# Kernel tuning notes

Measured on AMD Instinct MI355X. Metric: run time of the kernel, lower is better.

The kernel has to match this reference:

```python
import jax, jax.numpy as jnp
import numpy as np

N, E, DIN, DH, DC = 50000, 1600000, 128, 128, 40
EPS = 1e-5  # BatchNorm eps


def _seg_sum(v, idx, n):
    return jax.ops.segment_sum(v, idx, num_segments=n)


def setup_inputs() -> dict:
    key = jax.random.key(0)
    ks = jax.random.split(key, 24)
    rn = lambda i, shp, s=0.05: jax.random.normal(ks[i], shp, jnp.float32) * s
    return {
        "x": jax.random.normal(ks[0], (N, DIN), jnp.float32),
        "src": jax.random.randint(ks[1], (E,), 0, N, jnp.int32),
        "dst": jax.random.randint(ks[2], (E,), 0, N, jnp.int32),
        # CoNet layer 1 (in -> hidden)
        "w11s": rn(3, (DIN, DH)), "w11n": rn(4, (DIN, DH)), "b11": jnp.zeros((DH,), jnp.float32),
        "w12": rn(5, (DIN, DH)), "b12": jnp.zeros((DH,), jnp.float32),
        "w13": rn(6, (DIN, DH)), "a13l": rn(7, (DH,)), "a13r": rn(8, (DH,)), "b13": jnp.zeros((DH,), jnp.float32),
        "cw1": jax.random.uniform(ks[9], (3,), jnp.float32, 0.5, 1.5),
        # BatchNorm1d
        "g": jnp.ones((DH,), jnp.float32), "be": jnp.zeros((DH,), jnp.float32),
        # CoNet layer 2 (hidden -> out)
        "w21s": rn(10, (DH, DC)), "w21n": rn(11, (DH, DC)), "b21": jnp.zeros((DC,), jnp.float32),
        "w22": rn(12, (DH, DC)), "b22": jnp.zeros((DC,), jnp.float32),
        "w23": rn(13, (DH, DC)), "a23l": rn(14, (DC,)), "a23r": rn(15, (DC,)), "b23": jnp.zeros((DC,), jnp.float32),
        "cw2": jax.random.uniform(ks[16], (3,), jnp.float32, 0.5, 1.5),
    }


def conet(x, src, dst, ws, wn, bs, wg, bg, wa, al, ar, ba, cw):
    """AFFN CoNet: SAGE(mean) + GCN + GAT(1 head), fused by normalized weights."""
    n = x.shape[0]
    ones = jnp.ones((src.shape[0],), x.dtype)
    indeg = _seg_sum(ones, dst, n)   # in-degree per node
    outdeg = _seg_sum(ones, src, n)  # out-degree per node

    # --- SAGEConv, mean aggregator: fc_self(x) + fc_neigh(mean_neigh(x)) ---
    nei = _seg_sum(x[src], dst, n) / jnp.maximum(indeg, 1.0)[:, None]
    x1 = x @ ws + nei @ wn + bs

    ns = jnp.maximum(outdeg, 1.0) ** -0.5
    nd = jnp.maximum(indeg, 1.0) ** -0.5
    h = _seg_sum((x * ns[:, None])[src], dst, n) * nd[:, None]
    x2 = h @ wg + bg

    # --- GATConv, 1 head ---
    f = x @ wa                       # [N, out]
    el = f @ al                      # [N]
    er = f @ ar                      # [N]
    e = jax.nn.leaky_relu(el[src] + er[dst], 0.2)  # [E]
    m = jax.ops.segment_max(e, dst, num_segments=n)
    a = jnp.exp(e - m[dst])
    s = _seg_sum(a, dst, n)
    alpha = a / jnp.maximum(s[dst], 1e-9)
    x3 = _seg_sum(alpha[:, None] * f[src], dst, n) + ba

    w = cw / jnp.sum(cw)
    return w[0] * x1 + w[1] * x2 + w[2] * x3


def reference(x, src, dst,
              w11s, w11n, b11, w12, b12, w13, a13l, a13r, b13, cw1,
              g, be,
              w21s, w21n, b21, w22, b22, w23, a23l, a23r, b23, cw2):
    h = conet(x, src, dst, w11s, w11n, b11, w12, b12, w13, a13l, a13r, b13, cw1)
    # BatchNorm1d (training-mode batch statistics)
    mu = jnp.mean(h, axis=0)
    var = jnp.var(h, axis=0)
    h = (h - mu) * jax.lax.rsqrt(var + EPS) * g + be
    h = jax.nn.relu(h)
    # dropout in eval mode: identity
    h = conet(h, src, dst, w21s, w21n, b21, w22, b22, w23, a23l, a23r, b23, cw2)
    return jax.nn.log_softmax(h, axis=1)
```

## Files before the change

### kernel.cpp

```cpp
#include <hip/hip_runtime.h>
#include <hip/hip_bf16.h>
#include <math.h>

#define DIN 128
#define DH  128
#define DC  40

#define HCHUNK  12544
#define NSTRIPE 128
#define NPAD    (HCHUNK * 4)

typedef unsigned short u16;
typedef unsigned int u32;
typedef unsigned char u8;
typedef __attribute__((ext_vector_type(2))) float f32x2;
typedef __attribute__((ext_vector_type(4))) float f32x4;
typedef __attribute__((ext_vector_type(8))) short bf16x8;

static __device__ __forceinline__ float bf2f(u16 u) {
    union { u32 i; float f; } v; v.i = ((u32)u) << 16; return v.f;
}
static __device__ __forceinline__ u16 f2bf(float f) {
    __hip_bfloat16 h = __float2bfloat16(f);
    union { __hip_bfloat16 h; u16 u; } v; v.h = h; return v.u;
}
static __device__ __forceinline__ u32 pack2bf(float a, float b) {
    return ((u32)f2bf(b) << 16) | (u32)f2bf(a);
}

static __device__ __forceinline__ u8 f2fp8(float f) {
    u32 s = (__float_as_uint(f) >> 31) << 7;
    float a = fabsf(f);
    a = fminf(a, 448.f);
    if (a < 0.015625f) {
        int q = (int)rintf(a * 512.f);
        return (u8)(s | (u32)q);
    }
    u32 x = __float_as_uint(a);
    u32 lsb = (x >> 20) & 1;
    x += 0x0007FFFF + lsb;
    u32 e = (x >> 23) - 120;
    u32 m = (x >> 20) & 7;
    return (u8)(s | (e << 3) | m);
}

#if __has_builtin(__builtin_amdgcn_cvt_pk_f32_fp8)
template<bool HI>
static __device__ __forceinline__ f32x2 fp8pk(u32 w) {
    return __builtin_amdgcn_cvt_pk_f32_fp8((int)w, HI);
}
#else
static __device__ __forceinline__ float fp8dec1(u32 byte) {
    u32 s = (byte >> 7) & 1, em = byte & 0x7F;
    float v = __uint_as_float((s << 31) | (em << 20)) * 0x1p120f;
    return v;
}
template<bool HI>
static __device__ __forceinline__ f32x2 fp8pk(u32 w) {
    u32 b0 = HI ? ((w >> 16) & 0xff) : (w & 0xff);
    u32 b1 = HI ? ((w >> 24) & 0xff) : ((w >> 8) & 0xff);
    f32x2 r; r.x = fp8dec1(b0); r.y = fp8dec1(b1); return r;
}
#endif

__global__ __launch_bounds__(256) void k_prep(
        const float* w11s, const float* w11n, const float* w12, const float* w13,
        const float* b11, const float* b12, const float* b13, const float* cw1,
        const float* w21s, const float* w21n, const float* w22, const float* w23,
        const float* b21, const float* b22, const float* b23, const float* cw2,
        const float* a13l, const float* a13r, const float* a23l, const float* a23r,
        u16* __restrict__ Wf1, u16* __restrict__ Wf2,
        float* __restrict__ bc1, float* __restrict__ bc2, float* __restrict__ vattn,
        u32* __restrict__ zq, u32* __restrict__ zh) {
    int i = blockIdx.x * 256 + threadIdx.x;
    float s1 = cw1[0] + cw1[1] + cw1[2];
    float u0 = cw1[0] / s1, u1 = cw1[1] / s1, u2 = cw1[2] / s1;
    float s2 = cw2[0] + cw2[1] + cw2[2];
    float q0 = cw2[0] / s2, q1 = cw2[1] / s2, q2 = cw2[2] / s2;
    if (i < 65536) {
        int j = i & 7, lane = (i >> 3) & 63, nt = (i >> 9) & 7, kt = i >> 12;
        int k = kt * 32 + ((lane >> 4) << 3) + j;
        int n = nt * 16 + (lane & 15);
        float v;
        if (k < 128)      v = u0 * w11s[k * 128 + n];
        else if (k < 256) v = u0 * w11n[(k - 128) * 128 + n];
        else if (k < 384) v = u1 * w12[(k - 256) * 128 + n];
        else              v = u2 * w13[(k - 384) * 128 + n];
        Wf1[i] = f2bf(v);
    } else if (i < 90112) {
        int i2 = i - 65536;
        int j = i2 & 7;
        int l2 = i2 >> 3;
        int lane = l2 & 63;
        int t2 = l2 >> 6;
        int nt = t2 % 3, kt = t2 / 3;
        int k = kt * 32 + ((lane >> 4) << 3) + j;
        int n = nt * 16 + (lane & 15);
        float v = 0.f;
        if (n < 40) {
            if (k < 128)      v = q0 * w21s[k * 40 + n];
            else if (k < 256) v = q0 * w21n[(k - 128) * 40 + n];
            else if (k < 384) v = q1 * w22[(k - 256) * 40 + n];
            else              v = q2 * w23[(k - 384) * 40 + n];
        }
        Wf2[i2] = f2bf(v);
    } else if (i < 90624) {
        int t = i - 90112;
        if (t < 128) {
            float s = 0; for (int j = 0; j < 128; ++j) s += w13[t * 128 + j] * a13l[j];
            vattn[t] = s;
        } else if (t < 256) {
            int r = t - 128; float s = 0; for (int j = 0; j < 128; ++j) s += w13[r * 128 + j] * a13r[j];
            vattn[t] = s;
        } else if (t < 384) {
            int r = t - 256; float s = 0; for (int j = 0; j < 40; ++j) s += w23[r * 40 + j] * a23l[j];
            vattn[t] = s;
        } else {
            int r = t - 384; float s = 0; for (int j = 0; j < 40; ++j) s += w23[r * 40 + j] * a23r[j];
            vattn[t] = s;
        }
    } else if (i < 90752) {
        int c = i - 90624;
        bc1[c] = u0 * b11[c] + u1 * b12[c] + u2 * b13[c];
    } else if (i < 90792) {
        int c = i - 90752;
        bc2[c] = q0 * b21[c] + q1 * b22[c] + q2 * b23[c];
    } else if (i < 90856) {
        int t = i - 90792;
        if (t < 32) zq[t] = 0u; else zh[t - 32] = 0u;
    }
}

__global__ __launch_bounds__(256) void k_hist2(const int* __restrict__ src,
        const int* __restrict__ dst,
        u16* __restrict__ partialsS, u16* __restrict__ partialsD,
        u16* __restrict__ wsrank, int E, int eps) {
    __shared__ u32 histS[HCHUNK];
    __shared__ u32 histD[HCHUNK];
    int chunk = blockIdx.x;
    int stripe = blockIdx.y;
    int base = chunk * (HCHUNK * 2);
    for (int i = threadIdx.x; i < HCHUNK; i += 256) { histS[i] = 0; histD[i] = 0; }
    __syncthreads();
    int e0 = stripe * eps;
    int e1 = e0 + eps; if (e1 > E) e1 = E;
    for (int e = e0 + threadIdx.x; e < e1; e += 256) {
        int ks = src[e] - base;
        int kd = dst[e] - base;
        if ((u32)ks < (u32)(HCHUNK * 2))
            atomicAdd(&histS[ks >> 1], 1u << ((ks & 1) * 16));
        if ((u32)kd < (u32)(HCHUNK * 2)) {
            u32 old = atomicAdd(&histD[kd >> 1], 1u << ((kd & 1) * 16));
            wsrank[e] = (u16)((old >> ((kd & 1) * 16)) & 0xffff);
        }
    }
    __syncthreads();
    u32* prowS = (u32*)(partialsS + (size_t)stripe * NPAD + base);
    u32* prowD = (u32*)(partialsD + (size_t)stripe * NPAD + base);
    for (int i = threadIdx.x; i < HCHUNK; i += 256) { prowS[i] = histS[i]; prowD[i] = histD[i]; }
}

__global__ void k_pfx2(const u16* __restrict__ partialsS, u16* __restrict__ partialsD,
                       int* __restrict__ indeg, float* __restrict__ ns, int n) {
    int node = blockIdx.x * 256 + threadIdx.x;
    if (node >= NPAD) return;
    int runS = 0;
    for (int s0 = 0; s0 < NSTRIPE; s0 += 16) {
        u16 c[16];
#pragma unroll
        for (int i = 0; i < 16; ++i) c[i] = partialsS[(size_t)(s0 + i) * NPAD + node];
#pragma unroll
        for (int i = 0; i < 16; ++i) runS += c[i];
    }
    int runD = 0;
    for (int s0 = 0; s0 < NSTRIPE; s0 += 16) {
        u16 c[16];
#pragma unroll
        for (int i = 0; i < 16; ++i) c[i] = partialsD[(size_t)(s0 + i) * NPAD + node];
#pragma unroll
        for (int i = 0; i < 16; ++i) {
            partialsD[(size_t)(s0 + i) * NPAD + node] = (u16)runD;
            runD += c[i];
        }
    }
    if (node < n) {
        indeg[node] = runD;
        int d = runS < 1 ? 1 : runS;
        ns[node] = rsqrtf((float)d);
    }
}

__global__ void k_scan1(const int* __restrict__ deg, int* __restrict__ excl,
                        int* __restrict__ bsum, int n) {
    __shared__ int sh[256];
    int i = blockIdx.x * 256 + threadIdx.x;
    int v = (i < n) ? deg[i] : 0;
    sh[threadIdx.x] = v; __syncthreads();
    for (int o = 1; o < 256; o <<= 1) {
        int t = (threadIdx.x >= o) ? sh[threadIdx.x - o] : 0;
        __syncthreads(); sh[threadIdx.x] += t; __syncthreads();
    }
    if (i < n) excl[i] = sh[threadIdx.x] - v;
    if (threadIdx.x == 255) bsum[blockIdx.x] = sh[255];
}
__global__ void k_scan2(int* __restrict__ bsum, int nb) {
    __shared__ int sh[256];
    int t = threadIdx.x;
    int v = (t < nb) ? bsum[t] : 0;
    sh[t] = v; __syncthreads();
    for (int o = 1; o < 256; o <<= 1) {
        int u = (t >= o) ? sh[t - o] : 0;
        __syncthreads(); sh[t] += u; __syncthreads();
    }
    if (t < nb) bsum[t] = sh[t] - v;
}
__global__ void k_scan3(const int* __restrict__ excl, const int* __restrict__ bsum,
                        int* __restrict__ rowptr, int n, int E) {
    int i = blockIdx.x * 256 + threadIdx.x;
    if (i < n) rowptr[i] = excl[i] + bsum[blockIdx.x];
    if (i == 0) rowptr[n] = E;
}

__global__ __launch_bounds__(256) void k_place2(const int* __restrict__ src,
        const int* __restrict__ dst, const int* __restrict__ rowptr,
        const u16* __restrict__ partials, const u16* __restrict__ wsrank,
        int* __restrict__ col, int E, int eps) {
    int stripe = blockIdx.x;
    const u16* prow = partials + (size_t)stripe * NPAD;
    int sub = (eps + 3) >> 2;
    int e0 = stripe * eps + blockIdx.y * sub;
    int e1 = e0 + sub;
    int cap = stripe * eps + eps; if (cap > E) cap = E;
    if (e1 > cap) e1 = cap;
    for (int e = e0 + threadIdx.x; e < e1; e += 256) {
        int d = dst[e];
        col[rowptr[d] + prow[d] + wsrank[e]] = src[e];
    }
}

__global__ __launch_bounds__(256) void k_cvt_dots(const float* __restrict__ X,
        const float* __restrict__ vl, const float* __restrict__ vr, const float* __restrict__ ns,
        u16* __restrict__ Xb, u8* __restrict__ Xq,
        float2* __restrict__ elns, float* __restrict__ er, int n) {
    int w = (blockIdx.x * blockDim.x + threadIdx.x) >> 6;
    int lane = threadIdx.x & 63;
    if (w >= n) return;
    float2 xv = *(const float2*)&X[(size_t)w * 128 + lane * 2];
    *(u32*)&Xb[(size_t)w * 128 + lane * 2] = pack2bf(xv.x, xv.y);
    u16 q = (u16)f2fp8(xv.x) | ((u16)f2fp8(xv.y) << 8);
    *(u16*)&Xq[(size_t)w * 128 + lane * 2] = q;
    float2 a = *(const float2*)&vl[lane * 2];
    float2 b = *(const float2*)&vr[lane * 2];
    float dl = xv.x * a.x + xv.y * a.y;
    float dr = xv.x * b.x + xv.y * b.y;
    for (int off = 32; off; off >>= 1) {
        dl += __shfl_down(dl, off);
        dr += __shfl_down(dr, off);
    }
    if (lane == 0) { elns[w] = make_float2(dl, ns[w]); er[w] = dr; }
}

__global__ __launch_bounds__(256) void k_agg(const u8* __restrict__ Xq,
        const int* __restrict__ rowptr, const int* __restrict__ colsrc,
        const float2* __restrict__ elns, const float* __restrict__ er,
        u16* __restrict__ AG, int n) {
    int w = (blockIdx.x * blockDim.x + threadIdx.x) >> 6;
    int lane = threadIdx.x & 63;
    if (w >= n) return;
    int g = lane >> 4, gl = lane & 15;
    int beg = rowptr[w], end = rowptr[w + 1];
    int k = end - beg;
    float erd = er[w];
    f32x2 aS2[4] = {}, aG2[4] = {}, aA2[4] = {};
    float ssum = 0.f;
    for (int c0 = beg; c0 < end; c0 += 64) {
        int cnt = end - c0; if (cnt > 64) cnt = 64;
        int s = n; float p = 0.f; float nsl = 0.f;
        if (lane < cnt) {
            s = colsrc[c0 + lane];
            float2 v = elns[s];
            float t = v.x + erd;
            t = t > 0.f ? t : 0.2f * t;
            p = __expf(t);
            nsl = v.y;
        }
        float ps = p;
        for (int o = 32; o; o >>= 1) ps += __shfl_xor(ps, o);
        ssum += ps;
        int steps = (cnt + 3) >> 2;
#pragma unroll 8
        for (int t = 0; t < steps; ++t) {
            int j = (t << 2) + g;
            int sj = __shfl(s, j);
            float pj = __shfl(p, j);
            float nsj = __shfl(nsl, j);
            uint2 xq = *(const uint2*)&Xq[(size_t)sj * 128 + gl * 8];
            f32x2 xv2[4] = {fp8pk<false>(xq.x), fp8pk<true>(xq.x),
                            fp8pk<false>(xq.y), fp8pk<true>(xq.y)};
            f32x2 ns2 = {nsj, nsj}, p2 = {pj, pj};
#pragma unroll
            for (int q = 0; q < 4; ++q) {
                aS2[q] += xv2[q];
                aG2[q] += ns2 * xv2[q];
                aA2[q] += p2 * xv2[q];
            }
        }
    }
    float aS[8], aG[8], aA[8];
#pragma unroll
    for (int i = 0; i < 4; ++i) {
        aS[2 * i] = aS2[i][0]; aS[2 * i + 1] = aS2[i][1];
        aG[2 * i] = aG2[i][0]; aG[2 * i + 1] = aG2[i][1];
        aA[2 * i] = aA2[i][0]; aA[2 * i + 1] = aA2[i][1];
    }
#pragma unroll
    for (int i = 0; i < 8; ++i) {
        aS[i] += __shfl_xor(aS[i], 16); aS[i] += __shfl_xor(aS[i], 32);
        aG[i] += __shfl_xor(aG[i], 16); aG[i] += __shfl_xor(aG[i], 32);
        aA[i] += __shfl_xor(aA[i], 16); aA[i] += __shfl_xor(aA[i], 32);
    }
    int kc = k < 1 ? 1 : k;
    float invk = 1.f / (float)kc;
    float ndd = rsqrtf((float)kc);
    float gi = 1.f / fmaxf(ssum, 1e-9f);
    u16* row = AG + (size_t)w * 384;
    if (g == 0) {
        uint4 o = make_uint4(pack2bf(aS[0] * invk, aS[1] * invk), pack2bf(aS[2] * invk, aS[3] * invk),
                             pack2bf(aS[4] * invk, aS[5] * invk), pack2bf(aS[6] * invk, aS[7] * invk));
        *(uint4*)&row[gl * 8] = o;
    } else if (g == 1) {
        uint4 o = make_uint4(pack2bf(aG[0] * ndd, aG[1] * ndd), pack2bf(aG[2] * ndd, aG[3] * ndd),
                             pack2bf(aG[4] * ndd, aG[5] * ndd), pack2bf(aG[6] * ndd, aG[7] * ndd));
        *(uint4*)&row[128 + gl * 8] = o;
    } else if (g == 2) {
        uint4 o = make_uint4(pack2bf(aA[0] * gi, aA[1] * gi), pack2bf(aA[2] * gi, aA[3] * gi),
                             pack2bf(aA[4] * gi, aA[5] * gi), pack2bf(aA[6] * gi, aA[7] * gi));
        *(uint4*)&row[256 + gl * 8] = o;
    }
}

__global__ __launch_bounds__(256) void k_gemm1(const u16* __restrict__ Xb,
        const u16* __restrict__ AG, const u16* __restrict__ Wf,
        const float* __restrict__ bias, u16* __restrict__ C,
        float* __restrict__ bnacc, int M) {
    if (blockIdx.x == 0 && threadIdx.x < 256) bnacc[threadIdx.x] = 0.f;
    const int NT = 8;
    int wave = threadIdx.x >> 6;
    int lane = threadIdx.x & 63;
    int m0 = blockIdx.x * 64 + wave * 16;
    int arow = m0 + (lane & 15);
    if (arow >= M) arow = M - 1;
    int kq = lane >> 4;
    f32x4 acc[NT];
#pragma unroll
    for (int t = 0; t < NT; ++t) acc[t] = (f32x4){0.f, 0.f, 0.f, 0.f};
#pragma unroll
    for (int kt = 0; kt < 16; ++kt) {
        int k0 = kt * 32 + kq * 8;
        bf16x8 a;
        if (k0 < 128) a = *(const bf16x8*)&Xb[(size_t)arow * 128 + k0];
        else          a = *(const bf16x8*)&AG[(size_t)arow * 384 + (k0 - 128)];
        const u16* wb = Wf + ((size_t)kt * NT) * 512 + lane * 8;
#pragma unroll
        for (int t = 0; t < NT; ++t) {
            bf16x8 b = *(const bf16x8*)&wb[(size_t)t * 512];
            acc[t] = __builtin_amdgcn_mfma_f32_16x16x32_bf16(a, b, acc[t], 0, 0, 0);
        }
    }
    int ccol = lane & 15;
    int rbase = m0 + kq * 4;
#pragma unroll
    for (int t = 0; t < NT; ++t) {
        int col = t * 16 + ccol;
        float bv = bias[col];
#pragma unroll
        for (int r = 0; r < 4; ++r) {
            int rr = rbase + r;
            if (rr < M) C[(size_t)rr * 128 + col] = f2bf(acc[t][r] + bv);
        }
    }
}

__global__ __launch_bounds__(256) void k_gemm2_lsm(const u16* __restrict__ Xb,
        const u16* __restrict__ AG, const u16* __restrict__ Wf,
        const float* __restrict__ bias, float* __restrict__ out, int M) {
    const int NT = 3;
    int wave = threadIdx.x >> 6;
    int lane = threadIdx.x & 63;
    int m0 = blockIdx.x * 64 + wave * 16;
    int arow = m0 + (lane & 15);
    if (arow >= M) arow = M - 1;
    int kq = lane >> 4;
    f32x4 acc[NT];
#pragma unroll
    for (int t = 0; t < NT; ++t) acc[t] = (f32x4){0.f, 0.f, 0.f, 0.f};
#pragma unroll
    for (int kt = 0; kt < 16; ++kt) {
        int k0 = kt * 32 + kq * 8;
        bf16x8 a;
        if (k0 < 128) a = *(const bf16x8*)&Xb[(size_t)arow * 128 + k0];
        else          a = *(const bf16x8*)&AG[(size_t)arow * 384 + (k0 - 128)];
        const u16* wb = Wf + ((size_t)kt * NT) * 512 + lane * 8;
#pragma unroll
        for (int t = 0; t < NT; ++t) {
            bf16x8 b = *(const bf16x8*)&wb[(size_t)t * 512];
            acc[t] = __builtin_amdgcn_mfma_f32_16x16x32_bf16(a, b, acc[t], 0, 0, 0);
        }
    }
    int ccol = lane & 15;
    int rbase = m0 + kq * 4;
    bool valid[NT];
    float bv[NT];
#pragma unroll
    for (int t = 0; t < NT; ++t) {
        int col = t * 16 + ccol;
        valid[t] = (col < 40);
        bv[t] = valid[t] ? bias[col] : 0.f;
    }
#pragma unroll
    for (int r = 0; r < 4; ++r) {
        float v[NT];
#pragma unroll
        for (int t = 0; t < NT; ++t) v[t] = valid[t] ? (acc[t][r] + bv[t]) : -INFINITY;
        float mx = fmaxf(fmaxf(v[0], v[1]), v[2]);
        for (int o = 1; o < 16; o <<= 1) mx = fmaxf(mx, __shfl_xor(mx, o));
        float se = 0.f;
#pragma unroll
        for (int t = 0; t < NT; ++t) se += valid[t] ? __expf(v[t] - mx) : 0.f;
        for (int o = 1; o < 16; o <<= 1) se += __shfl_xor(se, o);
        float lse = mx + logf(se);
        int rr = rbase + r;
        if (rr < M) {
#pragma unroll
            for (int t = 0; t < NT; ++t) {
                int col = t * 16 + ccol;
                if (valid[t]) out[(size_t)rr * 40 + col] = v[t] - lse;
            }
        }
    }
}

__global__ __launch_bounds__(256) void k_bn_stats(const u16* __restrict__ H,
        float* __restrict__ acc, int nrows) {
    int c = threadIdx.x & 127;
    int rh = threadIdx.x >> 7;
    int r0 = blockIdx.x * 256;
    int rend = r0 + 256; if (rend > nrows) rend = nrows;
    float s = 0.f, q = 0.f;
    for (int r = r0 + rh; r < rend; r += 2) {
        float v = bf2f(H[(size_t)r * 128 + c]);
        s += v; q += v * v;
    }
    atomicAdd(&acc[c], s);
    atomicAdd(&acc[128 + c], q);
}

__global__ __launch_bounds__(256) void k_bnorm_dots(const u16* __restrict__ Hp,
        const float* __restrict__ bnacc, const float* __restrict__ g, const float* __restrict__ be,
        const float* __restrict__ vl, const float* __restrict__ vr,
        const float* __restrict__ ns,
        u16* __restrict__ H, u8* __restrict__ H8,
        float2* __restrict__ elns, float* __restrict__ er, float Nf, int n) {
    int w = (blockIdx.x * blockDim.x + threadIdx.x) >> 6;
    int lane = threadIdx.x & 63;
    if (w >= n) return;
    int c0 = lane * 2, c1 = lane * 2 + 1;
    float mu0 = bnacc[c0] / Nf, mu1 = bnacc[c1] / Nf;
    float var0 = bnacc[128 + c0] / Nf - mu0 * mu0;
    float var1 = bnacc[128 + c1] / Nf - mu1 * mu1;
    float sc0 = g[c0] * rsqrtf(var0 + 1e-5f);
    float sc1 = g[c1] * rsqrtf(var1 + 1e-5f);
    float sh0 = be[c0] - mu0 * sc0;
    float sh1 = be[c1] - mu1 * sc1;
    u32 hu = *(const u32*)&Hp[(size_t)w * 128 + lane * 2];
    float vx = bf2f((u16)hu), vy = bf2f((u16)(hu >> 16));
    float h0 = fmaxf(vx * sc0 + sh0, 0.f);
    float h1 = fmaxf(vy * sc1 + sh1, 0.f);
    *(u32*)&H[(size_t)w * 128 + lane * 2] = pack2bf(h0, h1);
    u16 q = (u16)f2fp8(h0) | ((u16)f2fp8(h1) << 8);
    *(u16*)&H8[(size_t)w * 128 + lane * 2] = q;
    float2 a = *(const float2*)&vl[lane * 2];
    float2 b = *(const float2*)&vr[lane * 2];
    float dl = h0 * a.x + h1 * a.y;
    float dr = h0 * b.x + h1 * b.y;
    for (int off = 32; off; off >>= 1) {
        dl += __shfl_down(dl, off);
        dr += __shfl_down(dr, off);
    }
    if (lane == 0) { elns[w] = make_float2(dl, ns[w]); er[w] = dr; }
}

extern "C" void kernel_launch(void* const* d_in, const int* in_sizes, int n_in,
                              void* d_out, int out_size, void* d_ws, size_t ws_size,
                              hipStream_t stream) {
    const float* x    = (const float*)d_in[0];
    const int*   src  = (const int*)d_in[1];
    const int*   dst  = (const int*)d_in[2];
    const float* w11s = (const float*)d_in[3];
    const float* w11n = (const float*)d_in[4];
    const float* b11  = (const float*)d_in[5];
    const float* w12  = (const float*)d_in[6];
    const float* b12  = (const float*)d_in[7];
    const float* w13  = (const float*)d_in[8];
    const float* a13l = (const float*)d_in[9];
    const float* a13r = (const float*)d_in[10];
    const float* b13  = (const float*)d_in[11];
    const float* cw1  = (const float*)d_in[12];
    const float* g    = (const float*)d_in[13];
    const float* be   = (const float*)d_in[14];
    const float* w21s = (const float*)d_in[15];
    const float* w21n = (const float*)d_in[16];
    const float* b21  = (const float*)d_in[17];
    const float* w22  = (const float*)d_in[18];
    const float* b22  = (const float*)d_in[19];
    const float* w23  = (const float*)d_in[20];
    const float* a23l = (const float*)d_in[21];
    const float* a23r = (const float*)d_in[22];
    const float* b23  = (const float*)d_in[23];
    const float* cw2  = (const float*)d_in[24];

    const int N = in_sizes[0] / DIN;
    const int E = in_sizes[1];

    char* ws = (char*)d_ws;
    size_t off = 0;
    auto alloc = [&](size_t bytes) { size_t o = off; off += (bytes + 255) & ~(size_t)255; return o; };
    u16*   Xb     = (u16*)(ws + alloc((size_t)N * 128 * 2));
    u8*    Xq     = (u8*)(ws + alloc((size_t)(N + 1) * 128));
    u16*   AG     = (u16*)(ws + alloc((size_t)N * 384 * 2));
    u16*   hpre   = (u16*)(ws + alloc((size_t)N * 128 * 2));
    u16*   h      = (u16*)(ws + alloc((size_t)N * 128 * 2));
    u8*    h8     = (u8*)(ws + alloc((size_t)(N + 1) * 128));
    int*   col    = (int*)(ws + alloc((size_t)E * 4));
    u16*   wsrank = (u16*)(ws + alloc((size_t)E * 2));
    u16*   partialsS = (u16*)(ws + alloc((size_t)NSTRIPE * NPAD * 2));
    u16*   partialsD = (u16*)(ws + alloc((size_t)NSTRIPE * NPAD * 2));
    int*   rowptr = (int*)(ws + alloc((size_t)(N + 1) * 4));
    int*   indeg  = (int*)(ws + alloc((size_t)N * 4));
    int*   excl   = (int*)(ws + alloc((size_t)N * 4));
    int*   bsum   = (int*)(ws + alloc(256 * 4));
    float* ns     = (float*)(ws + alloc((size_t)N * 4));
    float2* elns  = (float2*)(ws + alloc((size_t)N * 8));
    float* er     = (float*)(ws + alloc((size_t)N * 4));
    u16*   Wf1    = (u16*)(ws + alloc((size_t)16 * 8 * 64 * 8 * 2));
    u16*   Wf2    = (u16*)(ws + alloc((size_t)16 * 3 * 64 * 8 * 2));
    float* bc1    = (float*)(ws + alloc(128 * 4));
    float* bc2    = (float*)(ws + alloc(40 * 4));
    float* vattn  = (float*)(ws + alloc(512 * 4));
    float* bnacc  = (float*)(ws + alloc(256 * 4));

    int eb_eps = (E + NSTRIPE - 1) / NSTRIPE;
    int wb = (N * 64 + 255) / 256;
    int sb = (N + 255) / 256;
    int gb = (N + 63) / 64;
    int pb = (NPAD + 255) / 256;

    k_prep<<<(90856 + 255) / 256, 256, 0, stream>>>(
        w11s, w11n, w12, w13, b11, b12, b13, cw1,
        w21s, w21n, w22, w23, b21, b22, b23, cw2,
        a13l, a13r, a23l, a23r, Wf1, Wf2, bc1, bc2, vattn,
        (u32*)(Xq + (size_t)N * 128), (u32*)(h8 + (size_t)N * 128));

    {
        dim3 hg(2, NSTRIPE);
        k_hist2<<<hg, 256, 0, stream>>>(src, dst, partialsS, partialsD, wsrank, E, eb_eps);
        k_pfx2<<<pb, 256, 0, stream>>>(partialsS, partialsD, indeg, ns, N);
        k_scan1<<<sb, 256, 0, stream>>>(indeg, excl, bsum, N);
        k_scan2<<<1, 256, 0, stream>>>(bsum, sb);
        k_scan3<<<sb, 256, 0, stream>>>(excl, bsum, rowptr, N, E);
        dim3 pg(NSTRIPE, 4);
        k_place2<<<pg, 256, 0, stream>>>(src, dst, rowptr, partialsD, wsrank, col, E, eb_eps);
    }

    k_cvt_dots<<<wb, 256, 0, stream>>>(x, vattn, vattn + 128, ns, Xb, Xq, elns, er, N);
    k_agg<<<wb, 256, 0, stream>>>(Xq, rowptr, col, elns, er, AG, N);
    k_gemm1<<<gb, 256, 0, stream>>>(Xb, AG, Wf1, bc1, hpre, bnacc, N);

    k_bn_stats<<<(N + 255) / 256, 256, 0, stream>>>(hpre, bnacc, N);
    k_bnorm_dots<<<wb, 256, 0, stream>>>(hpre, bnacc, g, be, vattn + 256, vattn + 384, ns,
                                         h, h8, elns, er, (float)N, N);

    k_agg<<<wb, 256, 0, stream>>>(h8, rowptr, col, elns, er, AG, N);
    k_gemm2_lsm<<<gb, 256, 0, stream>>>(h, AG, Wf2, bc2, (float*)d_out, N);
}
```

Measured before the change: 424.4 us.

## Restructure degree histogram, fuse scan into prefix pass, fuse BN stats into GEMM

The degree histogram now covers all nodes in one block per stripe: byte counters for source degree, 16-bit counters for destination degree, and twice as many stripes. The first scan stage is folded into the prefix pass. The partial buffers reuse the AG and hpre workspaces. BatchNorm statistics are accumulated per block in the GEMM epilogue and reduced by one small kernel, which replaces the separate pass that re-read hpre. The GAT softmax denominator reduction is also hoisted out of the edge loop. The 8-bit source counters could overflow if a node has more than 255 out-edges within one stripe. The serial single-block reduction over all GEMM blocks adds a small tail.

```diff
diff --git a/kernel.cpp b/kernel.cpp
--- a/kernel.cpp
+++ b/kernel.cpp
@@ -6,9 +6,10 @@
 #define DH  128
 #define DC  40
 
-#define HCHUNK  12544
-#define NSTRIPE 128
-#define NPAD    (HCHUNK * 4)
+#define NSTRIPE 256
+#define NPAD    50176
+#define HD_WORDS (NPAD / 2)
+#define HS_WORDS (NPAD / 4)
 
 typedef unsigned short u16;
 typedef unsigned int u32;
@@ -133,40 +134,38 @@
 
 __global__ __launch_bounds__(256) void k_hist2(const int* __restrict__ src,
         const int* __restrict__ dst,
-        u16* __restrict__ partialsS, u16* __restrict__ partialsD,
+        u8* __restrict__ partialsS, u16* __restrict__ partialsD,
         u16* __restrict__ wsrank, int E, int eps) {
-    __shared__ u32 histS[HCHUNK];
-    __shared__ u32 histD[HCHUNK];
-    int chunk = blockIdx.x;
-    int stripe = blockIdx.y;
-    int base = chunk * (HCHUNK * 2);
-    for (int i = threadIdx.x; i < HCHUNK; i += 256) { histS[i] = 0; histD[i] = 0; }
+    __shared__ u32 histD[HD_WORDS];
+    __shared__ u32 histS[HS_WORDS];
+    int stripe = blockIdx.x;
+    for (int i = threadIdx.x; i < HD_WORDS; i += 256) histD[i] = 0;
+    for (int i = threadIdx.x; i < HS_WORDS; i += 256) histS[i] = 0;
     __syncthreads();
     int e0 = stripe * eps;
     int e1 = e0 + eps; if (e1 > E) e1 = E;
     for (int e = e0 + threadIdx.x; e < e1; e += 256) {
-        int ks = src[e] - base;
-        int kd = dst[e] - base;
-        if ((u32)ks < (u32)(HCHUNK * 2))
-            atomicAdd(&histS[ks >> 1], 1u << ((ks & 1) * 16));
-        if ((u32)kd < (u32)(HCHUNK * 2)) {
-            u32 old = atomicAdd(&histD[kd >> 1], 1u << ((kd & 1) * 16));
-            wsrank[e] = (u16)((old >> ((kd & 1) * 16)) & 0xffff);
-        }
+        int ks = src[e];
+        int kd = dst[e];
+        atomicAdd(&histS[ks >> 2], 1u << ((ks & 3) * 8));
+        u32 old = atomicAdd(&histD[kd >> 1], 1u << ((kd & 1) * 16));
+        wsrank[e] = (u16)((old >> ((kd & 1) * 16)) & 0xffff);
     }
     __syncthreads();
-    u32* prowS = (u32*)(partialsS + (size_t)stripe * NPAD + base);
-    u32* prowD = (u32*)(partialsD + (size_t)stripe * NPAD + base);
-    for (int i = threadIdx.x; i < HCHUNK; i += 256) { prowS[i] = histS[i]; prowD[i] = histD[i]; }
-}
-
-__global__ void k_pfx2(const u16* __restrict__ partialsS, u16* __restrict__ partialsD,
-                       int* __restrict__ indeg, float* __restrict__ ns, int n) {
+    u32* prowS = (u32*)(partialsS + (size_t)stripe * NPAD);
+    u32* prowD = (u32*)(partialsD + (size_t)stripe * NPAD);
+    for (int i = threadIdx.x; i < HD_WORDS; i += 256) prowD[i] = histD[i];
+    for (int i = threadIdx.x; i < HS_WORDS; i += 256) prowS[i] = histS[i];
+}
+
+__global__ __launch_bounds__(256) void k_pfx2(const u8* __restrict__ partialsS,
+        u16* __restrict__ partialsD,
+        int* __restrict__ excl, int* __restrict__ bsum,
+        float* __restrict__ ns, int n) {
     int node = blockIdx.x * 256 + threadIdx.x;
-    if (node >= NPAD) return;
     int runS = 0;
     for (int s0 = 0; s0 < NSTRIPE; s0 += 16) {
-        u16 c[16];
+        u8 c[16];
 #pragma unroll
         for (int i = 0; i < 16; ++i) c[i] = partialsS[(size_t)(s0 + i) * NPAD + node];
 #pragma unroll
@@ -184,25 +183,19 @@
         }
     }
     if (node < n) {
-        indeg[node] = runD;
         int d = runS < 1 ? 1 : runS;
         ns[node] = rsqrtf((float)d);
     }
-}
-
-__global__ void k_scan1(const int* __restrict__ deg, int* __restrict__ excl,
-                        int* __restrict__ bsum, int n) {
     __shared__ int sh[256];
-    int i = blockIdx.x * 256 + threadIdx.x;
-    int v = (i < n) ? deg[i] : 0;
-    sh[threadIdx.x] = v; __syncthreads();
+    sh[threadIdx.x] = runD; __syncthreads();
     for (int o = 1; o < 256; o <<= 1) {
         int t = (threadIdx.x >= o) ? sh[threadIdx.x - o] : 0;
         __syncthreads(); sh[threadIdx.x] += t; __syncthreads();
     }
-    if (i < n) excl[i] = sh[threadIdx.x] - v;
+    excl[node] = sh[threadIdx.x] - runD;
     if (threadIdx.x == 255) bsum[blockIdx.x] = sh[255];
 }
+
 __global__ void k_scan2(int* __restrict__ bsum, int nb) {
     __shared__ int sh[256];
     int t = threadIdx.x;
@@ -272,7 +265,7 @@
     int k = end - beg;
     float erd = er[w];
     f32x2 aS2[4] = {}, aG2[4] = {}, aA2[4] = {};
-    float ssum = 0.f;
+    float ssum_l = 0.f;
     for (int c0 = beg; c0 < end; c0 += 64) {
         int cnt = end - c0; if (cnt > 64) cnt = 64;
         int s = n; float p = 0.f; float nsl = 0.f;
@@ -284,9 +277,7 @@
             p = __expf(t);
             nsl = v.y;
         }
-        float ps = p;
-        for (int o = 32; o; o >>= 1) ps += __shfl_xor(ps, o);
-        ssum += ps;
+        ssum_l += p;
         int steps = (cnt + 3) >> 2;
 #pragma unroll 8
         for (int t = 0; t < steps; ++t) {
@@ -306,6 +297,7 @@
             }
         }
     }
+    for (int o = 32; o; o >>= 1) ssum_l += __shfl_xor(ssum_l, o);
     float aS[8], aG[8], aA[8];
 #pragma unroll
     for (int i = 0; i < 4; ++i) {
@@ -322,7 +314,7 @@
     int kc = k < 1 ? 1 : k;
     float invk = 1.f / (float)kc;
     float ndd = rsqrtf((float)kc);
-    float gi = 1.f / fmaxf(ssum, 1e-9f);
+    float gi = 1.f / fmaxf(ssum_l, 1e-9f);
     u16* row = AG + (size_t)w * 384;
     if (g == 0) {
         uint4 o = make_uint4(pack2bf(aS[0] * invk, aS[1] * invk), pack2bf(aS[2] * invk, aS[3] * invk),
@@ -342,8 +334,7 @@
 __global__ __launch_bounds__(256) void k_gemm1(const u16* __restrict__ Xb,
         const u16* __restrict__ AG, const u16* __restrict__ Wf,
         const float* __restrict__ bias, u16* __restrict__ C,
-        float* __restrict__ bnacc, int M) {
-    if (blockIdx.x == 0 && threadIdx.x < 256) bnacc[threadIdx.x] = 0.f;
+        float* __restrict__ bnpart, int M) {
     const int NT = 8;
     int wave = threadIdx.x >> 6;
     int lane = threadIdx.x & 63;
@@ -367,18 +358,45 @@
             acc[t] = __builtin_amdgcn_mfma_f32_16x16x32_bf16(a, b, acc[t], 0, 0, 0);
         }
     }
+    __shared__ float sS[128], sQ[128];
+    if (threadIdx.x < 128) { sS[threadIdx.x] = 0.f; sQ[threadIdx.x] = 0.f; }
+    __syncthreads();
     int ccol = lane & 15;
     int rbase = m0 + kq * 4;
 #pragma unroll
     for (int t = 0; t < NT; ++t) {
         int col = t * 16 + ccol;
         float bv = bias[col];
+        float cs = 0.f, cq = 0.f;
 #pragma unroll
         for (int r = 0; r < 4; ++r) {
             int rr = rbase + r;
-            if (rr < M) C[(size_t)rr * 128 + col] = f2bf(acc[t][r] + bv);
-        }
-    }
+            float v = acc[t][r] + bv;
+            if (rr < M) {
+                C[(size_t)rr * 128 + col] = f2bf(v);
+                cs += v; cq += v * v;
+            }
+        }
+        cs += __shfl_xor(cs, 16); cs += __shfl_xor(cs, 32);
+        cq += __shfl_xor(cq, 16); cq += __shfl_xor(cq, 32);
+        if (kq == 0) {
+            atomicAdd(&sS[col], cs);
+            atomicAdd(&sQ[col], cq);
+        }
+    }
+    __syncthreads();
+    if (threadIdx.x < 128) {
+        bnpart[(size_t)blockIdx.x * 256 + threadIdx.x] = sS[threadIdx.x];
+        bnpart[(size_t)blockIdx.x * 256 + 128 + threadIdx.x] = sQ[threadIdx.x];
+    }
+}
+
+__global__ void k_bn_reduce(const float* __restrict__ bnpart,
+                            float* __restrict__ bnacc, int nb) {
+    int c = threadIdx.x;
+    float s = 0.f;
+    for (int b = 0; b < nb; ++b) s += bnpart[(size_t)b * 256 + c];
+    bnacc[c] = s;
 }
 
 __global__ __launch_bounds__(256) void k_gemm2_lsm(const u16* __restrict__ Xb,
@@ -438,21 +456,6 @@
             }
         }
     }
-}
-
-__global__ __launch_bounds__(256) void k_bn_stats(const u16* __restrict__ H,
-        float* __restrict__ acc, int nrows) {
-    int c = threadIdx.x & 127;
-    int rh = threadIdx.x >> 7;
-    int r0 = blockIdx.x * 256;
-    int rend = r0 + 256; if (rend > nrows) rend = nrows;
-    float s = 0.f, q = 0.f;
-    for (int r = r0 + rh; r < rend; r += 2) {
-        float v = bf2f(H[(size_t)r * 128 + c]);
-        s += v; q += v * v;
-    }
-    atomicAdd(&acc[c], s);
-    atomicAdd(&acc[128 + c], q);
 }
 
 __global__ __launch_bounds__(256) void k_bnorm_dots(const u16* __restrict__ Hp,
@@ -533,11 +536,8 @@
     u8*    h8     = (u8*)(ws + alloc((size_t)(N + 1) * 128));
     int*   col    = (int*)(ws + alloc((size_t)E * 4));
     u16*   wsrank = (u16*)(ws + alloc((size_t)E * 2));
-    u16*   partialsS = (u16*)(ws + alloc((size_t)NSTRIPE * NPAD * 2));
-    u16*   partialsD = (u16*)(ws + alloc((size_t)NSTRIPE * NPAD * 2));
     int*   rowptr = (int*)(ws + alloc((size_t)(N + 1) * 4));
-    int*   indeg  = (int*)(ws + alloc((size_t)N * 4));
-    int*   excl   = (int*)(ws + alloc((size_t)N * 4));
+    int*   excl   = (int*)(ws + alloc((size_t)NPAD * 4));
     int*   bsum   = (int*)(ws + alloc(256 * 4));
     float* ns     = (float*)(ws + alloc((size_t)N * 4));
     float2* elns  = (float2*)(ws + alloc((size_t)N * 8));
@@ -548,12 +548,16 @@
     float* bc2    = (float*)(ws + alloc(40 * 4));
     float* vattn  = (float*)(ws + alloc(512 * 4));
     float* bnacc  = (float*)(ws + alloc(256 * 4));
-
-    int eb_eps = (E + NSTRIPE - 1) / NSTRIPE;
+    float* bnpart = (float*)(ws + alloc((size_t)((N + 63) / 64) * 256 * 4));
+
+    u8*  partialsS = (u8*)AG;
+    u16* partialsD = (u16*)hpre;
+
+    int eps = (E + NSTRIPE - 1) / NSTRIPE;
     int wb = (N * 64 + 255) / 256;
     int sb = (N + 255) / 256;
     int gb = (N + 63) / 64;
-    int pb = (NPAD + 255) / 256;
+    int pb = NPAD / 256;
 
     k_prep<<<(90856 + 255) / 256, 256, 0, stream>>>(
         w11s, w11n, w12, w13, b11, b12, b13, cw1,
@@ -561,22 +565,20 @@
         a13l, a13r, a23l, a23r, Wf1, Wf2, bc1, bc2, vattn,
         (u32*)(Xq + (size_t)N * 128), (u32*)(h8 + (size_t)N * 128));
 
+    k_hist2<<<NSTRIPE, 256, 0, stream>>>(src, dst, partialsS, partialsD, wsrank, E, eps);
+    k_pfx2<<<pb, 256, 0, stream>>>(partialsS, partialsD, excl, bsum, ns, N);
+    k_scan2<<<1, 256, 0, stream>>>(bsum, pb);
+    k_scan3<<<sb, 256, 0, stream>>>(excl, bsum, rowptr, N, E);
     {
-        dim3 hg(2, NSTRIPE);
-        k_hist2<<<hg, 256, 0, stream>>>(src, dst, partialsS, partialsD, wsrank, E, eb_eps);
-        k_pfx2<<<pb, 256, 0, stream>>>(partialsS, partialsD, indeg, ns, N);
-        k_scan1<<<sb, 256, 0, stream>>>(indeg, excl, bsum, N);
-        k_scan2<<<1, 256, 0, stream>>>(bsum, sb);
-        k_scan3<<<sb, 256, 0, stream>>>(excl, bsum, rowptr, N, E);
         dim3 pg(NSTRIPE, 4);
-        k_place2<<<pg, 256, 0, stream>>>(src, dst, rowptr, partialsD, wsrank, col, E, eb_eps);
+        k_place2<<<pg, 256, 0, stream>>>(src, dst, rowptr, partialsD, wsrank, col, E, eps);
     }
 
     k_cvt_dots<<<wb, 256, 0, stream>>>(x, vattn, vattn + 128, ns, Xb, Xq, elns, er, N);
     k_agg<<<wb, 256, 0, stream>>>(Xq, rowptr, col, elns, er, AG, N);
-    k_gemm1<<<gb, 256, 0, stream>>>(Xb, AG, Wf1, bc1, hpre, bnacc, N);
-
-    k_bn_stats<<<(N + 255) / 256, 256, 0, stream>>>(hpre, bnacc, N);
+    k_gemm1<<<gb, 256, 0, stream>>>(Xb, AG, Wf1, bc1, hpre, bnpart, N);
+
+    k_bn_reduce<<<1, 256, 0, stream>>>(bnpart, bnacc, gb);
     k_bnorm_dots<<<wb, 256, 0, stream>>>(hpre, bnacc, g, be, vattn + 256, vattn + 384, ns,
                                          h, h8, elns, er, (float)N, N);
 
```

After: 564.6 us. +33.0%, slower.
